# Kernel optimization log

Hardware: AMD Instinct MI355X
Metric: run time of the kernel (lower is better)

The kernel has to match this reference:

```python
import jax, jax.numpy as jnp
import numpy as np

B, C, V, K, H, W = 1, 3, 9, 8, 512, 512


def setup_inputs() -> dict:
    key = jax.random.key(0)
    k0, k1 = jax.random.split(key, 2)
    x = jax.random.normal(k0, (B, C, K, H, W), jnp.float32)          # FDL layers (spatial)
    y_views = jax.random.normal(k1, (B, C, V, H, W), jnp.float32)    # observed views (spatial)
    g = jnp.arange(3, dtype=jnp.float32) - 1.0                       # 3x3 camera grid positions
    uu, vv = jnp.meshgrid(g, g, indexing='ij')
    u = uu.reshape(-1)
    v = vv.reshape(-1)
    d = jnp.linspace(-2.0, 2.0, K).astype(jnp.float32)               # d_fdl disparities
    rho = jnp.full((1,), 0.3, jnp.float32)
    return {"x": x, "y_views": y_views, "u": u, "v": v, "d": d, "rho": rho}


def _pack_half_spectrum(Xf, x_c, y_c, n_proc):
    # [..., H, W] -> transpose to [..., W, H], center-roll so zero freq is at (x_c-1, y_c-1),
    # flatten x-major, keep the non-redundant half spectrum (first n_proc entries).
    Xt = jnp.swapaxes(Xf, -1, -2)
    Xt = jnp.roll(Xt, shift=(x_c - 1, y_c - 1), axis=(-2, -1))
    sh = Xt.shape
    return Xt.reshape(sh[:-2] + (sh[-2] * sh[-1],))[..., :n_proc]


def reference(x, y_views, u, v, d, rho):
    Bn, Cn, Kn = x.shape[0], x.shape[1], x.shape[2]
    Hn, Wn = x.shape[-2], x.shape[-1]
    rho = rho.reshape(())
    x_c = (Wn + 2) // 2                      # ceil((W+1)/2)
    y_c = (Hn + 2) // 2
    n_proc = Hn * (x_c - 1) + y_c            # half-spectrum size
    e0 = 1 - Hn % 2
    e1 = 1 - Wn % 2

    X = jnp.fft.fft2(x)                      # [B,C,K,H,W] complex64
    Y = jnp.fft.fft2(y_views)                # [B,C,V,H,W] complex64
    Xp = jnp.moveaxis(_pack_half_spectrum(X, x_c, y_c, n_proc), 2, 3) * rho   # [B,C,F,K]
    Yp = jnp.moveaxis(_pack_half_spectrum(Y, x_c, y_c, n_proc), 2, 3)         # [B,C,F,V]

    # centered angular frequency grids, flattened x-major to match packing order
    wx = (jnp.arange(Wn, dtype=jnp.float32) - (x_c - 1)) * (2.0 * np.pi / Wn)
    wy = (jnp.arange(Hn, dtype=jnp.float32) - (y_c - 1)) * (2.0 * np.pi / Hn)
    wx_f = jnp.repeat(wx, Hn)[:n_proc]       # [F]
    wy_f = jnp.tile(wy, Wn)[:n_proc]         # [F]

    # FDL data matrix A[f,v,k] = exp(i * d_k * (u_v*wx_f + v_v*wy_f))
    shift = u[None, :] * wx_f[:, None] + v[None, :] * wy_f[:, None]   # [F,V]
    A = jnp.exp(1j * shift[:, :, None] * d[None, None, :])            # [F,V,K] complex64
    Ah = jnp.conj(A)
    ATA = jnp.einsum('fvk,fvl->fkl', Ah, A)                           # [F,K,K]
    ATb = jnp.einsum('fvk,bcfv->bcfk', Ah, Yp)                        # [B,C,F,K]
    M = ATA + rho * jnp.eye(Kn, dtype=ATA.dtype)
    fdl = jnp.linalg.solve(M, (ATb + Xp)[..., None])[..., 0]          # [B,C,F,K]

    # pad redundant half with zeros, restore [B,C,K,H,W] layout
    fdl = jnp.pad(fdl, ((0, 0), (0, 0), (0, Hn * Wn - n_proc), (0, 0)))
    fdl = fdl.reshape(Bn, Cn, Wn, Hn, Kn).transpose(0, 1, 4, 3, 2)    # [B,C,K,H,W]

    # Hermitian (conjugate) symmetry reconstruction
    fdl = fdl.at[..., y_c:, x_c - 1:].set(jnp.conj(fdl[..., e0:y_c - 1, e1:x_c][..., ::-1, ::-1]))
    fdl = fdl.at[..., e0:y_c, x_c:].set(jnp.conj(fdl[..., y_c - 1:, e1:x_c - 1][..., ::-1, ::-1]))
    fdl = jnp.roll(fdl, shift=(1 - y_c, 1 - x_c), axis=(-2, -1))
    return jnp.fft.ifft2(fdl).real
```

## Files before the change

kernel.cpp:

```cpp
#include <hip/hip_runtime.h>
#include <math.h>

constexpr int N    = 512;
constexpr int LOGN = 9;
constexpr int NN   = N * N;
constexpr int CCH  = 3;
constexpr int KK   = 8;
constexpr int VV   = 9;
constexpr int FHALF = N * (N / 2) + (N / 2 + 1);
constexpr int NS   = 257;
constexpr float PI_F = 3.14159265358979323846f;

__device__ __forceinline__ float2 cmulf(float2 a, float2 b) {
    return make_float2(a.x * b.x - a.y * b.y, a.x * b.y + a.y * b.x);
}
__device__ __forceinline__ float2 cadd(float2 a, float2 b) { return make_float2(a.x + b.x, a.y + b.y); }
__device__ __forceinline__ float2 csub(float2 a, float2 b) { return make_float2(a.x - b.x, a.y - b.y); }

template<int SG>
__device__ __forceinline__ float2 cmuli(float2 z) {
    return (SG < 0) ? make_float2(z.y, -z.x) : make_float2(-z.y, z.x);
}

template<int SG>
__device__ __forceinline__ void dft8(float2 x[8]) {
    const float c = 0.70710678118654752440f;
    float2 a0 = cadd(x[0], x[4]), a1 = cadd(x[1], x[5]);
    float2 a2 = cadd(x[2], x[6]), a3 = cadd(x[3], x[7]);
    float2 d0 = csub(x[0], x[4]), d1 = csub(x[1], x[5]);
    float2 d2 = csub(x[2], x[6]), d3 = csub(x[3], x[7]);
    float2 b0 = d0;
    float2 b1 = cmulf(d1, make_float2(c, (float)SG * c));
    float2 b2 = cmuli<SG>(d2);
    float2 b3 = cmulf(d3, make_float2(-c, (float)SG * c));
    float2 aa0 = cadd(a0, a2), aa1 = cadd(a1, a3);
    float2 ab0 = csub(a0, a2), ab1 = cmuli<SG>(csub(a1, a3));
    float2 ba0 = cadd(b0, b2), ba1 = cadd(b1, b3);
    float2 bb0 = csub(b0, b2), bb1 = cmuli<SG>(csub(b1, b3));
    x[0] = cadd(aa0, aa1); x[4] = csub(aa0, aa1);
    x[2] = cadd(ab0, ab1); x[6] = csub(ab0, ab1);
    x[1] = cadd(ba0, ba1); x[5] = csub(ba0, ba1);
    x[3] = cadd(bb0, bb1); x[7] = csub(bb0, bb1);
}

__device__ __forceinline__ void twiddle8(float2 v[8], float base) {
    float sn, cs;
    __sincosf(base, &sn, &cs);
    float2 w1 = make_float2(cs, sn);
    float2 wk = w1;
    v[1] = cmulf(v[1], wk);
    #pragma unroll
    for (int k = 2; k < 8; ++k) { wk = cmulf(wk, w1); v[k] = cmulf(v[k], wk); }
}

template<int SG>
__device__ __forceinline__ void wave_fft512(float2 v[8], float* sre, float* sim,
                                            int t, int stride, int off) {
    int t1 = t >> 3, t0 = t & 7;
    dft8<SG>(v);
    twiddle8(v, (float)SG * (2.0f * PI_F / 512.0f) * (float)t);
    #pragma unroll
    for (int k = 0; k < 8; ++k) {
        int a = (68 * k + 8 * t1 + t0) * stride + off;
        sre[a] = v[k].x; sim[a] = v[k].y;
    }
    #pragma unroll
    for (int n = 0; n < 8; ++n) {
        int a = (68 * t1 + 8 * n + t0) * stride + off;
        v[n] = make_float2(sre[a], sim[a]);
    }
    dft8<SG>(v);
    twiddle8(v, (float)SG * (2.0f * PI_F / 64.0f) * (float)t0);
    #pragma unroll
    for (int k = 0; k < 8; ++k) {
        int a = (68 * t0 + 8 * k + t1) * stride + off;
        sre[a] = v[k].x; sim[a] = v[k].y;
    }
    #pragma unroll
    for (int n = 0; n < 8; ++n) {
        int a = (68 * n + 8 * t0 + t1) * stride + off;
        v[n] = make_float2(sre[a], sim[a]);
    }
    dft8<SG>(v);
}

__global__ __launch_bounds__(256) void k_fft_r2c_rows_pack_T(const float* __restrict__ inx,
                                                             const float* __restrict__ iny,
                                                             int nximg,
                                                             float2* __restrict__ outT) {
    __shared__ float ure[2313];
    __shared__ float uim[2313];
    int w = threadIdx.x >> 6, t = threadIdx.x & 63;
    int blk = blockIdx.x;
    int img = blk >> 6;
    int rowbase = (blk & 63) << 3;
    long long row0 = (long long)blk * 8 + 2 * w;
    long long xrows = (long long)nximg * N;
    const float* src0 = (row0 < xrows) ? (inx + row0 * N)
                                       : (iny + (row0 - xrows) * N);
    const float* src1 = src0 + N;
    float* sre = ure + w * 544;
    float* sim = uim + w * 544;
    float2 v[8];
    #pragma unroll
    for (int e = 0; e < 8; ++e) v[e] = make_float2(src0[t + 64 * e], src1[t + 64 * e]);
    wave_fft512<-1>(v, sre, sim, t, 1, 0);
    int kb = (t >> 3) + 8 * (t & 7);
    #pragma unroll
    for (int k0 = 0; k0 < 8; ++k0) {
        int p = kb + 64 * k0;
        sre[p] = v[k0].x; sim[p] = v[k0].y;
    }
    float2 r0v[4], r1v[4];
    #pragma unroll
    for (int k0 = 4; k0 < 8; ++k0) {
        int p  = kb + 64 * k0;
        int mp = 512 - p;
        float zmx = sre[mp], zmy = sim[mp];
        float2 Zp = v[k0];
        r0v[k0 - 4] = make_float2(0.5f * (Zp.x + zmx), 0.5f * (Zp.y - zmy));
        r1v[k0 - 4] = make_float2(0.5f * (Zp.y + zmy), 0.5f * (zmx - Zp.x));
    }
    float2 z0 = v[0];
    __syncthreads();
    #pragma unroll
    for (int k0 = 0; k0 < 4; ++k0) {
        int s = kb + 64 * k0;
        ure[s * 9 + 2 * w]     = r0v[k0].x; uim[s * 9 + 2 * w]     = r0v[k0].y;
        ure[s * 9 + 2 * w + 1] = r1v[k0].x; uim[s * 9 + 2 * w + 1] = r1v[k0].y;
    }
    if (t == 0) {
        ure[256 * 9 + 2 * w]     = z0.x; uim[256 * 9 + 2 * w]     = 0.0f;
        ure[256 * 9 + 2 * w + 1] = z0.y; uim[256 * 9 + 2 * w + 1] = 0.0f;
    }
    __syncthreads();
    float2* dst = outT + (long long)img * (NS * N);
    int tt = threadIdx.x;
    int r = tt & 7;
    #pragma unroll
    for (int j = 0; j < 8; ++j) {
        int s = j * 32 + (tt >> 3);
        dst[s * N + rowbase + r] = make_float2(ure[s * 9 + r], uim[s * 9 + r]);
    }
    if (tt < 8)
        dst[256 * N + rowbase + tt] = make_float2(ure[256 * 9 + tt], uim[256 * 9 + tt]);
}

__global__ __launch_bounds__(256) void k_fft_cols_lin(const float2* __restrict__ inT,
                                                      float2* __restrict__ out,
                                                      int nlines) {
    __shared__ float sre[4][544];
    __shared__ float sim[4][544];
    int w = threadIdx.x >> 6, t = threadIdx.x & 63;
    int l = blockIdx.x * 4 + w;
    if (l >= nlines) return;
    int img = l / NS;
    int s   = l - img * NS;
    const float2* src = inT + (long long)img * (NS * N) + (long long)s * N;
    float2 v[8];
    #pragma unroll
    for (int e = 0; e < 8; ++e) v[e] = src[t + 64 * e];
    wave_fft512<-1>(v, sre[w], sim[w], t, 1, 0);
    int outrow = (s == 256) ? 256 : s;
    float2* dst = out + (long long)img * NN + (long long)outrow * N;
    int kb = (t >> 3) + 8 * (t & 7);
    #pragma unroll
    for (int k0 = 0; k0 < 8; ++k0) dst[kb + 64 * (k0 ^ 4)] = v[k0];
}

__global__ __launch_bounds__(256) void k_fft_r2c_rows(const float* __restrict__ in,
                                                      float2* __restrict__ out) {
    __shared__ float sre[4][544];
    __shared__ float sim[4][544];
    int w = threadIdx.x >> 6, t = threadIdx.x & 63;
    long long grow = (long long)blockIdx.x * 4 + w;
    const float* src = in + grow * N;
    float2 v[8];
    #pragma unroll
    for (int e = 0; e < 8; ++e) v[e] = make_float2(src[t + 64 * e], 0.0f);
    wave_fft512<-1>(v, sre[w], sim[w], t, 1, 0);
    float2* dst = out + grow * N;
    int kb = (t >> 3) + 8 * (t & 7);
    #pragma unroll
    for (int k0 = 0; k0 < 8; ++k0) dst[kb + 64 * k0] = v[k0];
}

template<int SG>
__global__ __launch_bounds__(256) void k_fft_pairswap(float2* __restrict__ data,
                                                      float scale, int lex, int sex) {
    __shared__ float sre[4][544];
    __shared__ float sim[4][544];
    int w = threadIdx.x >> 6, t = threadIdx.x & 63;
    int b = blockIdx.x;
    long long imgBase = (long long)(b >> 7) * NN;
    int pa = (b & 127) << 1;
    int rowg = pa + (w & 1) + ((w >> 1) << 8);
    const float2* src = data + imgBase + (long long)rowg * N;
    float2 v[8];
    #pragma unroll
    for (int e = 0; e < 8; ++e) v[e] = src[t + 64 * (e ^ lex)];
    __syncthreads();
    wave_fft512<SG>(v, sre[w], sim[w], t, 1, 0);
    float2* dst = data + imgBase + (long long)(rowg ^ 256) * N;
    int kb = (t >> 3) + 8 * (t & 7);
    #pragma unroll
    for (int k0 = 0; k0 < 8; ++k0) {
        float2 z = v[k0];
        dst[kb + 64 * (k0 ^ sex)] = make_float2(z.x * scale, z.y * scale);
    }
}

__device__ __forceinline__ void accum_pair(float2 bacc[KK], float tr[KK], float s,
                                           float d0, float dlt, float2 Yp, float2 Yn) {
    float2 Sp = make_float2(Yp.x + Yn.x, Yp.y + Yn.y);
    float2 Dm = make_float2(Yp.x - Yn.x, Yp.y - Yn.y);
    float sn, cs;
    __sincosf(s * d0, &sn, &cs);  float2 p = make_float2(cs, sn);
    __sincosf(s * dlt, &sn, &cs); float2 q = make_float2(cs, sn);
    float2 w = q;
    #pragma unroll
    for (int k = 0; k < KK; ++k) {
        bacc[k].x += p.x * Sp.x + p.y * Dm.y;
        bacc[k].y += p.x * Sp.y - p.y * Dm.x;
        if (k < KK - 1) {
            p = cmulf(p, q);
            tr[k + 1] += 2.0f * w.x;
            w = cmulf(w, q);
        }
    }
}

__device__ __forceinline__ void solve_point(float2 bacc[KK], float tr[KK], float rho) {
    float diag = tr[0] + rho;
    float L[36], Li[KK];
    #pragma unroll
    for (int j = 0; j < KK; ++j) {
        float acc = diag;
        #pragma unroll
        for (int t = 0; t < j; ++t) { float l = L[(j * (j - 1)) / 2 + t]; acc -= l * l; }
        float dj = sqrtf(acc);
        float inv = 1.0f / dj;
        Li[j] = inv;
        #pragma unroll
        for (int i = j + 1; i < KK; ++i) {
            float a = tr[i - j];
            #pragma unroll
            for (int t = 0; t < j; ++t)
                a -= L[(i * (i - 1)) / 2 + t] * L[(j * (j - 1)) / 2 + t];
            L[(i * (i - 1)) / 2 + j] = a * inv;
        }
    }
    #pragma unroll
    for (int i = 0; i < KK; ++i) {
        float2 a = bacc[i];
        #pragma unroll
        for (int t = 0; t < i; ++t) {
            float l = L[(i * (i - 1)) / 2 + t];
            a.x -= l * bacc[t].x;
            a.y -= l * bacc[t].y;
        }
        bacc[i] = make_float2(a.x * Li[i], a.y * Li[i]);
    }
    #pragma unroll
    for (int i = KK - 1; i >= 0; --i) {
        float2 a = bacc[i];
        #pragma unroll
        for (int t = i + 1; t < KK; ++t) {
            float l = L[(t * (t - 1)) / 2 + i];
            a.x -= l * bacc[t].x;
            a.y -= l * bacc[t].y;
        }
        bacc[i] = make_float2(a.x * Li[i], a.y * Li[i]);
    }
}

__global__ __launch_bounds__(256) void k_solve_ifft(const float2* __restrict__ Xs,
                                                    const float2* __restrict__ Ys,
                                                    float2* __restrict__ P,
                                                    float2* __restrict__ S0,
                                                    const float* __restrict__ uu,
                                                    const float* __restrict__ vv,
                                                    const float* __restrict__ dd,
                                                    const float* __restrict__ rhop) {
    __shared__ float gre[KK][N];
    __shared__ float gim[KK][N];
    __shared__ float fsre[4][544];
    __shared__ float fsim[4][544];
    int a  = blockIdx.x;
    int ch = blockIdx.y;
    int t  = threadIdx.x;
    float rho = rhop[0];
    float d0 = dd[0], dlt = dd[1] - dd[0];
    const float C = 2.0f * PI_F / (float)N;
    float wxv = (float)(a - 256) * C;
    const float2* Xrow = Xs + (long long)ch * KK * NN + (long long)a * N;
    const float2* Yrow = Ys + (long long)ch * VV * NN + (long long)a * N;
    float wy0 = (float)(t - 256) * C;
    float wy1 = (float)(t)       * C;

    float2 bacc0[KK], bacc1[KK];
    float tr0[KK], tr1[KK];
    {
        const float2* Yc = Yrow + (long long)4 * NN;
        float2 yc0 = Yc[t], yc1 = Yc[t + 256];
        #pragma unroll
        for (int k = 0; k < KK; ++k) { bacc0[k] = yc0; bacc1[k] = yc1; }
        tr0[0] = tr1[0] = (float)VV;
        #pragma unroll
        for (int l = 1; l < KK; ++l) { tr0[l] = 1.0f; tr1[l] = 1.0f; }
    }
    #pragma unroll
    for (int j = 0; j < 4; ++j) {
        int vp = 5 + j, vn = 3 - j;
        float su = uu[vp], sv = vv[vp];
        const float2* Ypr = Yrow + (long long)vp * NN;
        const float2* Ynr = Yrow + (long long)vn * NN;
        float2 Yp0 = Ypr[t], Yn0 = Ynr[t];
        float2 Yp1 = Ypr[t + 256], Yn1 = Ynr[t + 256];
        accum_pair(bacc0, tr0, su * wxv + sv * wy0, d0, dlt, Yp0, Yn0);
        accum_pair(bacc1, tr1, su * wxv + sv * wy1, d0, dlt, Yp1, Yn1);
    }
    #pragma unroll
    for (int k = 0; k < KK; ++k) {
        const float2* Xr = Xrow + (long long)k * NN;
        float2 x0v = Xr[t], x1v = Xr[t + 256];
        bacc0[k].x += rho * x0v.x; bacc0[k].y += rho * x0v.y;
        bacc1[k].x += rho * x1v.x; bacc1[k].y += rho * x1v.y;
    }
    solve_point(bacc0, tr0, rho);
    solve_point(bacc1, tr1, rho);
    #pragma unroll
    for (int k = 0; k < KK; ++k) {
        gre[k][t] = bacc0[k].x;       gim[k][t] = bacc0[k].y;
        gre[k][t + 256] = bacc1[k].x; gim[k][t + 256] = bacc1[k].y;
    }
    __syncthreads();
    if (a == 256 && t >= 1) {
        int b = t + 256, bs = 256 - t;
        #pragma unroll
        for (int k = 0; k < KK; ++k) {
            gre[k][b] = gre[k][bs];
            gim[k][b] = -gim[k][bs];
        }
    }
    __syncthreads();

    int w = t >> 6, lane = t & 63;
    int kb = (lane >> 3) + 8 * (lane & 7);
    const float inv512 = 1.0f / 512.0f;
    #pragma unroll
    for (int r = 0; r < 2; ++r) {
        int k = (w << 1) | r;
        float2 v[8];
        #pragma unroll
        for (int e = 0; e < 8; ++e) {
            int idx = (lane + 64 * e) ^ 256;
            v[e] = make_float2(gre[k][idx], gim[k][idx]);
        }
        wave_fft512<1>(v, fsre[w], fsim[w], lane, 1, 0);
        float s0x = gre[k][0], s0y = gim[k][0];
        if (lane == 0)
            S0[(long long)(ch * KK + k) * 257 + a] =
                make_float2(s0x * inv512, s0y * inv512);
        float2* Pimg = P + (long long)(ch * KK + k) * NN;
        int prow = (a >= 1 && a <= 255) ? (a + 256) : (a == 0 ? 256 : 0);
        float2* pmain = Pimg + (long long)prow * N;
        #pragma unroll
        for (int k0 = 0; k0 < 8; ++k0) {
            int pos = kb + 64 * k0;
            float2 W = v[k0];
            pmain[pos] = make_float2(W.x * inv512, W.y * inv512);
        }
    }
}

__global__ __launch_bounds__(256) void k_fft_cols_inv_real(const float2* __restrict__ in,
                                                           const float2* __restrict__ T0,
                                                           float* __restrict__ out,
                                                           float scale) {
    __shared__ float tre[4896];
    __shared__ float tim[4896];
    int t = threadIdx.x;
    long long imgOff = (long long)blockIdx.y * NN;
    int b0 = blockIdx.x << 3;
    {
        int xi2 = (t & 3) << 1;
        int yb  = t >> 2;
        const float2* img = in + imgOff;
        const float2* T0i = T0 + (long long)blockIdx.y * 257;
        #pragma unroll
        for (int it = 0; it < 4; ++it) {
            int p = 256 + it * 64 + yb;
            float4 q = *(const float4*)&img[(long long)p * N + b0 + xi2];
            int c = p * 9 + xi2;
            tre[c] = q.x; tim[c] = q.y; tre[c + 1] = q.z; tim[c + 1] = q.w;
            if (p > 256) {
                float2 t0 = T0i[p - 256];
                int m0 = b0 + xi2;
                float sg0 = (m0 & 1) ? -1.0f : 1.0f;
                float sg1 = -sg0;
                int cm = (512 - p) * 9 + xi2;
                tre[cm]     = q.x - t0.x * sg0;
                tim[cm]     = -q.y + t0.y * sg0;
                tre[cm + 1] = q.z - t0.x * sg1;
                tim[cm + 1] = -q.w + t0.y * sg1;
            }
        }
        if (t < 4) {
            int xi2b = t << 1;
            float4 q = *(const float4*)&img[(long long)(b0 + xi2b)];
            tre[xi2b] = q.x; tim[xi2b] = q.y; tre[xi2b + 1] = q.z; tim[xi2b + 1] = q.w;
        }
    }
    __syncthreads();
    int w = t >> 6, lane = t & 63;
    int kb = (lane >> 3) + 8 * (lane & 7);
    #pragma unroll
    for (int r = 0; r < 2; ++r) {
        int cc = (w << 1) | r;
        float2 v[8];
        #pragma unroll
        for (int e = 0; e < 8; ++e) {
            int a = (lane + 64 * e) * 9 + cc;
            v[e] = make_float2(tre[a], tim[a]);
        }
        wave_fft512<1>(v, tre, tim, lane, 9, cc);
        #pragma unroll
        for (int k0 = 0; k0 < 8; ++k0)
            tre[(kb + 64 * k0) * 9 + cc] = v[k0].x;
    }
    __syncthreads();
    {
        int xi = t >> 5, co = t & 31;
        float* orow = out + (long long)blockIdx.y * NN + (long long)(b0 + xi) * N;
        #pragma unroll
        for (int it = 0; it < 4; ++it) {
            int ww = it * 128 + co * 4;
            *(float4*)&orow[ww] = make_float4(tre[ww * 9 + xi] * scale,
                                              tre[(ww + 1) * 9 + xi] * scale,
                                              tre[(ww + 2) * 9 + xi] * scale,
                                              tre[(ww + 3) * 9 + xi] * scale);
        }
    }
}

__global__ __launch_bounds__(256) void k_transpose_inplace(float2* __restrict__ data) {
    int ti = blockIdx.x, tj = blockIdx.y;
    if (ti > tj) return;
    float2* img = data + (long long)blockIdx.z * NN;
    __shared__ float2 ta[32][33];
    __shared__ float2 tb[32][33];
    int tx = threadIdx.x, ty = threadIdx.y;
    int r0 = ti << 5, c0 = tj << 5;
    bool diag = (ti == tj);
    #pragma unroll
    for (int kk = 0; kk < 4; ++kk) {
        int r = ty + (kk << 3);
        ta[r][tx] = img[(long long)(r0 + r) * N + (c0 + tx)];
        if (!diag) tb[r][tx] = img[(long long)(c0 + r) * N + (r0 + tx)];
    }
    __syncthreads();
    #pragma unroll
    for (int kk = 0; kk < 4; ++kk) {
        int r = ty + (kk << 3);
        img[(long long)(c0 + r) * N + (r0 + tx)] = ta[tx][r];
        if (!diag) img[(long long)(r0 + r) * N + (c0 + tx)] = tb[tx][r];
    }
}

__global__ __launch_bounds__(256) void k_fft_c2r_rows(const float2* __restrict__ in,
                                                      float* __restrict__ out, float scale) {
    __shared__ float sre[4][544];
    __shared__ float sim[4][544];
    int w = threadIdx.x >> 6, t = threadIdx.x & 63;
    long long grow = (long long)blockIdx.x * 4 + w;
    const float2* src = in + grow * N;
    float2 v[8];
    #pragma unroll
    for (int e = 0; e < 8; ++e) v[e] = src[t + 64 * e];
    wave_fft512<1>(v, sre[w], sim[w], t, 1, 0);
    float* dst = out + grow * N;
    int kb = (t >> 3) + 8 * (t & 7);
    #pragma unroll
    for (int k0 = 0; k0 < 8; ++k0) dst[kb + 64 * k0] = v[k0].x * scale;
}

__global__ __launch_bounds__(256) void k_solve(float2* __restrict__ Xs,
                                               const float2* __restrict__ Ys,
                                               const float* __restrict__ uu,
                                               const float* __restrict__ vv,
                                               const float* __restrict__ dd,
                                               const float* __restrict__ rhop) {
    int f = blockIdx.x * 256 + threadIdx.x;
    if (f >= FHALF) return;
    long long coffX = (long long)blockIdx.y * KK * NN;
    long long coffY = (long long)blockIdx.y * VV * NN;
    float rho = rhop[0];
    int x = f >> LOGN;
    int y = f & (N - 1);
    float wxv = (float)(x - N / 2) * (2.0f * PI_F / (float)N);
    float wyv = (float)(y - N / 2) * (2.0f * PI_F / (float)N);
    float d0 = dd[0], dlt = dd[1] - dd[0];
    float2 bacc[KK];
    float tr[KK];
    {
        float2 Yc = Ys[coffY + (long long)4 * NN + f];
        #pragma unroll
        for (int k = 0; k < KK; ++k) bacc[k] = Yc;
        tr[0] = (float)VV;
        #pragma unroll
        for (int l = 1; l < KK; ++l) tr[l] = 1.0f;
    }
    #pragma unroll
    for (int j = 0; j < 4; ++j) {
        int vp = 5 + j, vn = 3 - j;
        float s = uu[vp] * wxv + vv[vp] * wyv;
        accum_pair(bacc, tr, s, d0, dlt,
                   Ys[coffY + (long long)vp * NN + f],
                   Ys[coffY + (long long)vn * NN + f]);
    }
    #pragma unroll
    for (int k = 0; k < KK; ++k) {
        float2 Xk = Xs[coffX + (long long)k * NN + f];
        bacc[k].x += rho * Xk.x;
        bacc[k].y += rho * Xk.y;
    }
    solve_point(bacc, tr, rho);
    int xm = (N - x) & (N - 1);
    int ym = (N - y) & (N - 1);
    long long fm = (long long)xm * N + ym;
    bool conjMirror = false, zeroMirror = false;
    if (x >= 1 && x <= N / 2 - 1) {
        if (y == 0) zeroMirror = true; else conjMirror = true;
    } else if (x == N / 2 && y >= 1 && y <= N / 2 - 1) {
        conjMirror = true;
    }
    #pragma unroll
    for (int k = 0; k < KK; ++k) {
        float2* base = Xs + coffX + (long long)k * NN;
        float2 z = bacc[k];
        base[f] = z;
        if (conjMirror)      base[fm] = make_float2(z.x, -z.y);
        else if (zeroMirror) base[fm] = make_float2(0.f, 0.f);
    }
}

extern "C" void kernel_launch(void* const* d_in, const int* in_sizes, int n_in,
                              void* d_out, int out_size, void* d_ws, size_t ws_size,
                              hipStream_t stream) {
    (void)in_sizes; (void)n_in; (void)out_size;
    const float* x   = (const float*)d_in[0];
    const float* yv  = (const float*)d_in[1];
    const float* uu  = (const float*)d_in[2];
    const float* vvp = (const float*)d_in[3];
    const float* dd  = (const float*)d_in[4];
    const float* rho = (const float*)d_in[5];
    float* out = (float*)d_out;
    float2* ws = (float2*)d_ws;

    const size_t s0Elems = (size_t)CCH * KK * 257;
    const size_t needBatchedPack =
        (size_t)2 * CCH * (KK + VV) * NN * sizeof(float2) + s0Elems * sizeof(float2);
    const size_t needChanPack =
        (size_t)2 * (KK + VV) * NN * sizeof(float2) + (size_t)KK * 257 * sizeof(float2);
    const float invN = 1.0f / (float)N;

    if (ws_size >= needChanPack) {
        bool batched = ws_size >= needBatchedPack;
        int iters = batched ? 1 : CCH;
        int ncs   = batched ? CCH : 1;
        int nx = ncs * KK, ny = ncs * VV;
        for (int it = 0; it < iters; ++it) {
            float2* Xt = ws;
            float2* Yt = ws + (size_t)nx * NN;
            float2* Rt = ws + (size_t)(nx + ny) * NN;
            float2* S0 = ws + (size_t)2 * (nx + ny) * NN;
            const float* xin = x  + (size_t)it * KK * NN;
            const float* yin = yv + (size_t)it * VV * NN;
            float* oout = out + (size_t)it * KK * NN;
            int nlines = (nx + ny) * NS;
            k_fft_r2c_rows_pack_T<<<(nx + ny) * 64, 256, 0, stream>>>(xin, yin, nx, Rt);
            k_fft_cols_lin<<<(nlines + 3) / 4, 256, 0, stream>>>(Rt, Xt, nlines);
            k_solve_ifft<<<dim3(257, ncs), 256, 0, stream>>>(Xt, Yt, Rt, S0, uu, vvp, dd, rho);
            k_fft_cols_inv_real<<<dim3(N / 8, nx), 256, 0, stream>>>(Rt, S0, oout, invN);
        }
    } else {
        for (int it = 0; it < CCH; ++it) {
            float2* Xb = ws;
            float2* Yb = ws + (size_t)KK * NN;
            const float* xin = x  + (size_t)it * KK * NN;
            const float* yin = yv + (size_t)it * VV * NN;
            float* oout = out + (size_t)it * KK * NN;
            k_fft_r2c_rows<<<KK * (N / 4), 256, 0, stream>>>(xin, Xb);
            k_fft_r2c_rows<<<VV * (N / 4), 256, 0, stream>>>(yin, Yb);
            k_transpose_inplace<<<dim3(16, 16, KK), dim3(32, 8), 0, stream>>>(Xb);
            k_transpose_inplace<<<dim3(16, 16, VV), dim3(32, 8), 0, stream>>>(Yb);
            k_fft_pairswap<-1><<<KK * (N / 4), 256, 0, stream>>>(Xb, 1.0f, 0, 4);
            k_fft_pairswap<-1><<<VV * (N / 4), 256, 0, stream>>>(Yb, 1.0f, 0, 4);
            k_solve<<<dim3((FHALF + 255) / 256, 1), 256, 0, stream>>>(Xb, Yb, uu, vvp, dd, rho);
            k_fft_pairswap<1><<<KK * (N / 4), 256, 0, stream>>>(Xb, invN, 4, 0);
            k_transpose_inplace<<<dim3(16, 16, KK), dim3(32, 8), 0, stream>>>(Xb);
            k_fft_c2r_rows<<<KK * (N / 4), 256, 0, stream>>>(Xb, oout, invN);
        }
    }
}
```

Before: 168.4 us.

## Fuse forward column FFT into the per-frequency solve kernel

Removes the separate column-FFT kernel that wrote full spectra for the X and Y images to global memory. The solve kernel now loads each transposed row line, runs the 512-point FFT in shared memory, and uses the result directly for the solve and the inverse FFT. This removes one launch and a full write and read of the intermediate spectra. In exchange, the shared memory footprint grows (a 9x512 float2 buffer), which may lower occupancy, and the grid of 257xC blocks now does more serial FFT work per block.

```diff
diff --git a/kernel.cpp b/kernel.cpp
--- a/kernel.cpp
+++ b/kernel.cpp
@@ -134,7 +134,7 @@
         ure[256 * 9 + 2 * w + 1] = z0.y; uim[256 * 9 + 2 * w + 1] = 0.0f;
     }
     __syncthreads();
-    float2* dst = outT + (long long)img * (NS * N);
+    float2* dst = outT + (long long)img * ((long long)NS * N);
     int tt = threadIdx.x;
     int r = tt & 7;
     #pragma unroll
@@ -144,28 +144,6 @@
     }
     if (tt < 8)
         dst[256 * N + rowbase + tt] = make_float2(ure[256 * 9 + tt], uim[256 * 9 + tt]);
-}
-
-__global__ __launch_bounds__(256) void k_fft_cols_lin(const float2* __restrict__ inT,
-                                                      float2* __restrict__ out,
-                                                      int nlines) {
-    __shared__ float sre[4][544];
-    __shared__ float sim[4][544];
-    int w = threadIdx.x >> 6, t = threadIdx.x & 63;
-    int l = blockIdx.x * 4 + w;
-    if (l >= nlines) return;
-    int img = l / NS;
-    int s   = l - img * NS;
-    const float2* src = inT + (long long)img * (NS * N) + (long long)s * N;
-    float2 v[8];
-    #pragma unroll
-    for (int e = 0; e < 8; ++e) v[e] = src[t + 64 * e];
-    wave_fft512<-1>(v, sre[w], sim[w], t, 1, 0);
-    int outrow = (s == 256) ? 256 : s;
-    float2* dst = out + (long long)img * NN + (long long)outrow * N;
-    int kb = (t >> 3) + 8 * (t & 7);
-    #pragma unroll
-    for (int k0 = 0; k0 < 8; ++k0) dst[kb + 64 * (k0 ^ 4)] = v[k0];
 }
 
 __global__ __launch_bounds__(256) void k_fft_r2c_rows(const float* __restrict__ in,
@@ -274,35 +252,53 @@
     }
 }
 
-__global__ __launch_bounds__(256) void k_solve_ifft(const float2* __restrict__ Xs,
-                                                    const float2* __restrict__ Ys,
-                                                    float2* __restrict__ P,
-                                                    float2* __restrict__ S0,
-                                                    const float* __restrict__ uu,
-                                                    const float* __restrict__ vv,
-                                                    const float* __restrict__ dd,
-                                                    const float* __restrict__ rhop) {
-    __shared__ float gre[KK][N];
-    __shared__ float gim[KK][N];
+__global__ __launch_bounds__(256) void k_fused_solve(const float2* __restrict__ Rt,
+                                                     float2* __restrict__ P,
+                                                     float2* __restrict__ S0,
+                                                     int nximg,
+                                                     const float* __restrict__ uu,
+                                                     const float* __restrict__ vvp,
+                                                     const float* __restrict__ dd,
+                                                     const float* __restrict__ rhop) {
+    __shared__ float2 buf[VV][N];
     __shared__ float fsre[4][544];
     __shared__ float fsim[4][544];
     int a  = blockIdx.x;
     int ch = blockIdx.y;
     int t  = threadIdx.x;
+    int w = t >> 6, lane = t & 63;
+    int kb = (lane >> 3) + 8 * (lane & 7);
+    const long long LN = (long long)NS * N;
+
+    {
+        int ybase = nximg + ch * VV;
+        #pragma unroll
+        for (int rep = 0; rep < 3; ++rep) {
+            int vimg = w + 4 * rep;
+            if (vimg < VV) {
+                const float2* src = Rt + (long long)(ybase + vimg) * LN + (long long)a * N;
+                float2 fv[8];
+                #pragma unroll
+                for (int e = 0; e < 8; ++e) fv[e] = src[lane + 64 * e];
+                wave_fft512<-1>(fv, fsre[w], fsim[w], lane, 1, 0);
+                #pragma unroll
+                for (int k0 = 0; k0 < 8; ++k0)
+                    buf[vimg][kb + 64 * (k0 ^ 4)] = fv[k0];
+            }
+        }
+    }
+    __syncthreads();
+
     float rho = rhop[0];
     float d0 = dd[0], dlt = dd[1] - dd[0];
     const float C = 2.0f * PI_F / (float)N;
     float wxv = (float)(a - 256) * C;
-    const float2* Xrow = Xs + (long long)ch * KK * NN + (long long)a * N;
-    const float2* Yrow = Ys + (long long)ch * VV * NN + (long long)a * N;
     float wy0 = (float)(t - 256) * C;
     float wy1 = (float)(t)       * C;
-
     float2 bacc0[KK], bacc1[KK];
     float tr0[KK], tr1[KK];
     {
-        const float2* Yc = Yrow + (long long)4 * NN;
-        float2 yc0 = Yc[t], yc1 = Yc[t + 256];
+        float2 yc0 = buf[4][t], yc1 = buf[4][t + 256];
         #pragma unroll
         for (int k = 0; k < KK; ++k) { bacc0[k] = yc0; bacc1[k] = yc1; }
         tr0[0] = tr1[0] = (float)VV;
@@ -312,18 +308,31 @@
     #pragma unroll
     for (int j = 0; j < 4; ++j) {
         int vp = 5 + j, vn = 3 - j;
-        float su = uu[vp], sv = vv[vp];
-        const float2* Ypr = Yrow + (long long)vp * NN;
-        const float2* Ynr = Yrow + (long long)vn * NN;
-        float2 Yp0 = Ypr[t], Yn0 = Ynr[t];
-        float2 Yp1 = Ypr[t + 256], Yn1 = Ynr[t + 256];
+        float su = uu[vp], sv = vvp[vp];
+        float2 Yp0 = buf[vp][t],       Yn0 = buf[vn][t];
+        float2 Yp1 = buf[vp][t + 256], Yn1 = buf[vn][t + 256];
         accum_pair(bacc0, tr0, su * wxv + sv * wy0, d0, dlt, Yp0, Yn0);
         accum_pair(bacc1, tr1, su * wxv + sv * wy1, d0, dlt, Yp1, Yn1);
     }
+    __syncthreads();
+
+    #pragma unroll
+    for (int r = 0; r < 2; ++r) {
+        int k = (w << 1) | r;
+        const float2* src = Rt + (long long)(ch * KK + k) * LN + (long long)a * N;
+        float2 fv[8];
+        #pragma unroll
+        for (int e = 0; e < 8; ++e) fv[e] = src[lane + 64 * e];
+        wave_fft512<-1>(fv, fsre[w], fsim[w], lane, 1, 0);
+        #pragma unroll
+        for (int k0 = 0; k0 < 8; ++k0)
+            buf[k][kb + 64 * (k0 ^ 4)] = fv[k0];
+    }
+    __syncthreads();
+
     #pragma unroll
     for (int k = 0; k < KK; ++k) {
-        const float2* Xr = Xrow + (long long)k * NN;
-        float2 x0v = Xr[t], x1v = Xr[t + 256];
+        float2 x0v = buf[k][t], x1v = buf[k][t + 256];
         bacc0[k].x += rho * x0v.x; bacc0[k].y += rho * x0v.y;
         bacc1[k].x += rho * x1v.x; bacc1[k].y += rho * x1v.y;
     }
@@ -331,37 +340,33 @@
     solve_point(bacc1, tr1, rho);
     #pragma unroll
     for (int k = 0; k < KK; ++k) {
-        gre[k][t] = bacc0[k].x;       gim[k][t] = bacc0[k].y;
-        gre[k][t + 256] = bacc1[k].x; gim[k][t + 256] = bacc1[k].y;
+        buf[k][t]       = bacc0[k];
+        buf[k][t + 256] = bacc1[k];
     }
     __syncthreads();
     if (a == 256 && t >= 1) {
         int b = t + 256, bs = 256 - t;
         #pragma unroll
         for (int k = 0; k < KK; ++k) {
-            gre[k][b] = gre[k][bs];
-            gim[k][b] = -gim[k][bs];
-        }
-    }
-    __syncthreads();
-
-    int w = t >> 6, lane = t & 63;
-    int kb = (lane >> 3) + 8 * (lane & 7);
+            float2 z = buf[k][bs];
+            buf[k][b] = make_float2(z.x, -z.y);
+        }
+    }
+    __syncthreads();
+
     const float inv512 = 1.0f / 512.0f;
     #pragma unroll
     for (int r = 0; r < 2; ++r) {
         int k = (w << 1) | r;
         float2 v[8];
         #pragma unroll
-        for (int e = 0; e < 8; ++e) {
-            int idx = (lane + 64 * e) ^ 256;
-            v[e] = make_float2(gre[k][idx], gim[k][idx]);
-        }
+        for (int e = 0; e < 8; ++e)
+            v[e] = buf[k][(lane + 64 * e) ^ 256];
         wave_fft512<1>(v, fsre[w], fsim[w], lane, 1, 0);
-        float s0x = gre[k][0], s0y = gim[k][0];
+        float2 s0 = buf[k][0];
         if (lane == 0)
             S0[(long long)(ch * KK + k) * 257 + a] =
-                make_float2(s0x * inv512, s0y * inv512);
+                make_float2(s0.x * inv512, s0.y * inv512);
         float2* Pimg = P + (long long)(ch * KK + k) * NN;
         int prow = (a >= 1 && a <= 255) ? (a + 256) : (a == 0 ? 256 : 0);
         float2* pmain = Pimg + (long long)prow * N;
@@ -558,31 +563,31 @@
     float* out = (float*)d_out;
     float2* ws = (float2*)d_ws;
 
-    const size_t s0Elems = (size_t)CCH * KK * 257;
-    const size_t needBatchedPack =
-        (size_t)2 * CCH * (KK + VV) * NN * sizeof(float2) + s0Elems * sizeof(float2);
-    const size_t needChanPack =
-        (size_t)2 * (KK + VV) * NN * sizeof(float2) + (size_t)KK * 257 * sizeof(float2);
     const float invN = 1.0f / (float)N;
-
-    if (ws_size >= needChanPack) {
-        bool batched = ws_size >= needBatchedPack;
+    const size_t lnPer = (size_t)NS * N;
+    const size_t needBatched =
+        ((size_t)CCH * (KK + VV) * lnPer + (size_t)CCH * KK * NN
+         + (size_t)CCH * KK * 257) * sizeof(float2);
+    const size_t needChan =
+        ((size_t)(KK + VV) * lnPer + (size_t)KK * NN
+         + (size_t)KK * 257) * sizeof(float2);
+
+    if (ws_size >= needChan) {
+        bool batched = ws_size >= needBatched;
         int iters = batched ? 1 : CCH;
         int ncs   = batched ? CCH : 1;
         int nx = ncs * KK, ny = ncs * VV;
         for (int it = 0; it < iters; ++it) {
-            float2* Xt = ws;
-            float2* Yt = ws + (size_t)nx * NN;
-            float2* Rt = ws + (size_t)(nx + ny) * NN;
-            float2* S0 = ws + (size_t)2 * (nx + ny) * NN;
+            float2* Rt = ws;
+            float2* P  = ws + (size_t)(nx + ny) * lnPer;
+            float2* S0 = P  + (size_t)nx * NN;
             const float* xin = x  + (size_t)it * KK * NN;
             const float* yin = yv + (size_t)it * VV * NN;
             float* oout = out + (size_t)it * KK * NN;
-            int nlines = (nx + ny) * NS;
             k_fft_r2c_rows_pack_T<<<(nx + ny) * 64, 256, 0, stream>>>(xin, yin, nx, Rt);
-            k_fft_cols_lin<<<(nlines + 3) / 4, 256, 0, stream>>>(Rt, Xt, nlines);
-            k_solve_ifft<<<dim3(257, ncs), 256, 0, stream>>>(Xt, Yt, Rt, S0, uu, vvp, dd, rho);
-            k_fft_cols_inv_real<<<dim3(N / 8, nx), 256, 0, stream>>>(Rt, S0, oout, invN);
+            k_fused_solve<<<dim3(257, ncs), 256, 0, stream>>>(Rt, P, S0, nx,
+                                                              uu, vvp, dd, rho);
+            k_fft_cols_inv_real<<<dim3(N / 8, nx), 256, 0, stream>>>(P, S0, oout, invN);
         }
     } else {
         for (int it = 0; it < CCH; ++it) {
```

Measured after the change: 181.2 us. 7.6% more time.
